# Optimization experiments

Measured on AMD Instinct MI355X. Metric: run time of the kernel, lower is better.

Reference implementation:

```python
import jax, jax.numpy as jnp
import numpy as np

N_HEAD = 16
SCALE = True


def setup_inputs() -> dict:
    key = jax.random.key(0)
    k1, k2, k3 = jax.random.split(key, 3)
    B, S, D = 4, 2048, 1024
    x = jax.random.normal(k1, (B, S, D), dtype=jnp.float32)
    w_attn = jax.random.normal(k2, (D, 3 * D), dtype=jnp.float32) * 0.02
    b_attn = jnp.zeros((3 * D,), dtype=jnp.float32)
    w_proj = jax.random.normal(k3, (D, D), dtype=jnp.float32) * 0.02
    b_proj = jnp.zeros((D,), dtype=jnp.float32)
    return {"x": x, "w_attn": w_attn, "b_attn": b_attn, "w_proj": w_proj, "b_proj": b_proj}


def reference(x, w_attn, b_attn, w_proj, b_proj):
    B, S, D = x.shape
    H = N_HEAD
    hd = D // H
    qkv = x @ w_attn + b_attn  # [B,S,3D] (Conv1D)
    q, k, v = jnp.split(qkv, 3, axis=-1)
    # split heads -> [B,H,S,hd]
    q = q.reshape(B, S, H, hd).transpose(0, 2, 1, 3)
    k = k.reshape(B, S, H, hd).transpose(0, 2, 1, 3)
    v = v.reshape(B, S, H, hd).transpose(0, 2, 1, 3)
    w = jnp.einsum('bhqd,bhkd->bhqk', q, k)  # [B,H,S,S]
    if SCALE:
        w = w / jnp.sqrt(jnp.asarray(hd, dtype=w.dtype))
    # causal mask exactly as in source: w*b + -10000*(1-b)
    bmask = jnp.tril(jnp.ones((S, S), dtype=w.dtype))[None, None]
    w = w * bmask + (-10000.0) * (1.0 - bmask)
    w = jax.nn.softmax(w, axis=-1)
    a = jnp.einsum('bhqk,bhkd->bhqd', w, v)  # [B,H,S,hd]
    a = a.transpose(0, 2, 1, 3).reshape(B, S, D)  # merge heads
    out = a @ w_proj + b_proj
    return out
```

## Files before the change

kernel.cpp:

```cpp
#include <hip/hip_runtime.h>

typedef __attribute__((ext_vector_type(8))) _Float16 f16x8;
typedef __attribute__((ext_vector_type(2))) __fp16 h16x2;
typedef __attribute__((ext_vector_type(4))) float f32x4;

#define S_LEN 2048
#define DMODEL 1024
#define NHEAD 16
#define HD 64
#define QKV_LD 3072
#define BTOT 4
#define LOG2E 1.4426950408889634f

#define GLL16(g, l)                                              \
  __builtin_amdgcn_global_load_lds(                              \
      (const __attribute__((address_space(1))) void*)(g),        \
      (__attribute__((address_space(3))) void*)(l), 16, 0, 0)

#define MFMA16(a, b, c) __builtin_amdgcn_mfma_f32_16x16x32_f16(a, b, c, 0, 0, 0)

__global__ __launch_bounds__(256) void cvt_f32_f16_k(const float* __restrict__ in,
                                                     _Float16* __restrict__ out, int n) {
  int i = (blockIdx.x * 256 + threadIdx.x) * 4;
  int stride = gridDim.x * 256 * 4;
  for (; i < n; i += stride) {
    float4 v = *(const float4*)(in + i);
    _Float16 h[4];
    h[0] = (_Float16)v.x; h[1] = (_Float16)v.y; h[2] = (_Float16)v.z; h[3] = (_Float16)v.w;
    *(uint2*)(out + i) = *(const uint2*)h;
  }
}

__global__ __launch_bounds__(256) void transpose_cvt_k(const float* __restrict__ W,
                                                       _Float16* __restrict__ Wt,
                                                       int K, int N) {
  __shared__ float t[32][33];
  int n0 = blockIdx.x * 32, k0 = blockIdx.y * 32;
  int tx = threadIdx.x, ty = threadIdx.y;
#pragma unroll
  for (int i = 0; i < 32; i += 8)
    t[ty + i][tx] = W[(size_t)(k0 + ty + i) * N + n0 + tx];
  __syncthreads();
#pragma unroll
  for (int i = 0; i < 32; i += 8)
    Wt[(size_t)(n0 + ty + i) * K + k0 + tx] = (_Float16)t[tx][ty + i];
}

template <int OUT_F32>
__global__ __launch_bounds__(256) void gemm_bt_k(const _Float16* __restrict__ A,
                                                 const _Float16* __restrict__ Bt,
                                                 const float* __restrict__ bias,
                                                 void* __restrict__ C,
                                                 int M, int N, int K) {
  __shared__ _Float16 As[128 * 64];
  __shared__ _Float16 Bs[128 * 64];
  const int tid = threadIdx.x;
  const int wid = tid >> 6, lane = tid & 63;
  const int quad = lane >> 4, l16 = lane & 15;
  const int wr = wid >> 1, wc = wid & 1;

  const int lin = blockIdx.y * gridDim.x + blockIdx.x;
  const int width = 8 * gridDim.x;
  const int group = lin / width;
  const int pm = group * 8 + (lin % width) % 8;
  const int pn = (lin % width) / 8;
  const int tm = pm * 128, tn = pn * 128;

  const int row0 = tid >> 3;
  const int xc = 8 * ((tid & 7) ^ (row0 & 7));
  const _Float16* Ag = A + (size_t)(tm + row0) * K + xc;
  const _Float16* Bg = Bt + (size_t)(tn + row0) * K + xc;
  _Float16* AsW = &As[wid * 512];
  _Float16* BsW = &Bs[wid * 512];

  f32x4 acc[4][4] = {};

  for (int k0 = 0; k0 < K; k0 += 64) {
    __syncthreads();
#pragma unroll
    for (int p = 0; p < 4; p++) {
      GLL16(Ag + k0 + (size_t)(32 * p) * K, AsW + 2048 * p);
      GLL16(Bg + k0 + (size_t)(32 * p) * K, BsW + 2048 * p);
    }
    __syncthreads();

#pragma unroll
    for (int ks = 0; ks < 2; ks++) {
      f16x8 af[4], bf[4];
#pragma unroll
      for (int mt = 0; mt < 4; mt++)
        af[mt] = *(const f16x8*)&As[(wr * 64 + mt * 16 + l16) * 64 +
                                    (((ks * 4 + quad) ^ (l16 & 7)) << 3)];
#pragma unroll
      for (int nt = 0; nt < 4; nt++)
        bf[nt] = *(const f16x8*)&Bs[(wc * 64 + nt * 16 + l16) * 64 +
                                    (((ks * 4 + quad) ^ (l16 & 7)) << 3)];
#pragma unroll
      for (int mt = 0; mt < 4; mt++)
#pragma unroll
        for (int nt = 0; nt < 4; nt++)
          acc[mt][nt] = MFMA16(af[mt], bf[nt], acc[mt][nt]);
    }
  }

#pragma unroll
  for (int nt = 0; nt < 4; nt++) {
    int col = tn + wc * 64 + nt * 16 + l16;
    float bv = bias[col];
#pragma unroll
    for (int mt = 0; mt < 4; mt++) {
      int row = tm + wr * 64 + mt * 16 + quad * 4;
#pragma unroll
      for (int r = 0; r < 4; r++) {
        float v = acc[mt][nt][r] + bv;
        if (OUT_F32)
          ((float*)C)[(size_t)(row + r) * N + col] = v;
        else
          ((_Float16*)C)[(size_t)(row + r) * N + col] = (_Float16)v;
      }
    }
  }
}

__global__ __launch_bounds__(256, 3) void attn_k(const _Float16* __restrict__ qkv,
                                                 _Float16* __restrict__ out) {
  __shared__ _Float16 Ks[2][4096];
  __shared__ _Float16 VTs[2][4096];
  __shared__ _Float16 Ps[4][2304];

  const int tid = threadIdx.x, wid = tid >> 6, lane = tid & 63;
  const int quad = lane >> 4, l16 = lane & 15;
  const int bh = blockIdx.x, b = bh >> 4, h = bh & 15;
  const int tile = 15 - blockIdx.y;
  const int qt = tile * 128;
  const _Float16* base = qkv + (size_t)b * S_LEN * QKV_LD + h * HD;

  const int krow = tid >> 3;
  const _Float16* Kg = base + DMODEL + (size_t)krow * QKV_LD +
                       8 * ((tid & 7) ^ (krow & 7));
  const int kp = tid & 31, dbase = (tid >> 5) * 8;
  const _Float16* Vg = base + 2 * DMODEL + (size_t)(2 * kp) * QKV_LD + dbase;

  int voff[8];
#pragma unroll
  for (int i = 0; i < 8; i++) {
    int d = dbase + i;
    voff[i] = d * 32 + (((kp >> 2) ^ (d & 7)) << 2) + (kp & 3);
  }

  auto stage_V = [&](int bufi, uint4 v0, uint4 v1) {
    union { uint4 u; _Float16 h[8]; } a, c;
    a.u = v0; c.u = v1;
    uint* VT32 = (uint*)VTs[bufi];
#pragma unroll
    for (int i = 0; i < 8; i++) {
      union { _Float16 h[2]; uint u; } w;
      w.h[0] = a.h[i]; w.h[1] = c.h[i];
      VT32[voff[i]] = w.u;
    }
  };

  f16x8 bq[2][2];
  {
    const _Float16 qs = (_Float16)(0.125f * LOG2E);
#pragma unroll
    for (int nt = 0; nt < 2; nt++)
#pragma unroll
      for (int ks = 0; ks < 2; ks++) {
        union { uint4 u; f16x8 h; } v;
        v.u = *(const uint4*)(base + (size_t)(qt + wid * 32 + nt * 16 + l16) * QKV_LD +
                              ks * 32 + quad * 8);
        bq[nt][ks] = v.h * qs;
      }
  }

  float m_i[2] = {-1e30f, -1e30f}, l_i[2] = {0.f, 0.f};
  f32x4 o[4][2] = {};

  const int qmin_w = qt + wid * 32;
  const int qmax_w = qmin_w + 31;
  const int nj = qt / 64 + 2;

  GLL16(Kg, &Ks[0][wid * 512]);
  GLL16(Kg + (size_t)32 * QKV_LD, &Ks[0][2048 + wid * 512]);
  stage_V(0, *(const uint4*)(Vg), *(const uint4*)(Vg + QKV_LD));
  __syncthreads();

  for (int j = 0; j < nj; j++) {
    const int cur = j & 1, nxt = cur ^ 1;
    const int k0g = j * 64;
    const bool pf = (j + 1 < nj);
    uint4 pv0, pv1;
    if (pf) {
      const int kn = k0g + 64;
      GLL16(Kg + (size_t)kn * QKV_LD, &Ks[nxt][wid * 512]);
      GLL16(Kg + (size_t)(kn + 32) * QKV_LD, &Ks[nxt][2048 + wid * 512]);
      pv0 = *(const uint4*)(Vg + (size_t)kn * QKV_LD);
      pv1 = *(const uint4*)(Vg + (size_t)(kn + 1) * QKV_LD);
    }

    if (k0g <= qmax_w) {
      f32x4 sc[4][2] = {};
#pragma unroll
      for (int ks = 0; ks < 2; ks++) {
#pragma unroll
        for (int mt = 0; mt < 4; mt++) {
          f16x8 ak = *(const f16x8*)&Ks[cur][(mt * 16 + l16) * 64 +
                                             (((ks * 4 + quad) ^ (l16 & 7)) << 3)];
          sc[mt][0] = MFMA16(ak, bq[0][ks], sc[mt][0]);
          sc[mt][1] = MFMA16(ak, bq[1][ks], sc[mt][1]);
        }
      }

      const bool need_mask = (k0g + 63 > qmin_w);
      float s[2][16];
      float mx[2];
#pragma unroll
      for (int nt = 0; nt < 2; nt++) {
        const int qg = qmin_w + nt * 16 + l16;
#pragma unroll
        for (int mt = 0; mt < 4; mt++)
#pragma unroll
          for (int r = 0; r < 4; r++) {
            float v = sc[mt][nt][r];
            if (need_mask) {
              int kg = k0g + mt * 16 + quad * 4 + r;
              v = (kg <= qg) ? v : -3.0e38f;
            }
            s[nt][mt * 4 + r] = v;
          }
        float t0 = fmaxf(fmaxf(s[nt][0], s[nt][1]), s[nt][2]);
        float t1 = fmaxf(fmaxf(s[nt][3], s[nt][4]), s[nt][5]);
        float t2 = fmaxf(fmaxf(s[nt][6], s[nt][7]), s[nt][8]);
        float t3 = fmaxf(fmaxf(s[nt][9], s[nt][10]), s[nt][11]);
        float t4 = fmaxf(fmaxf(s[nt][12], s[nt][13]), s[nt][14]);
        float m0 = fmaxf(fmaxf(t0, t1), t2);
        float m1 = fmaxf(fmaxf(t3, t4), s[nt][15]);
        float m = fmaxf(m0, m1);
        m = fmaxf(m, __shfl_xor(m, 16, 64));
        m = fmaxf(m, __shfl_xor(m, 32, 64));
        mx[nt] = m;
      }

      bool grow = (mx[0] > m_i[0] + 8.0f) || (mx[1] > m_i[1] + 8.0f);
      if (__any(grow)) {
#pragma unroll
        for (int nt = 0; nt < 2; nt++) {
          float mnew = fmaxf(m_i[nt], mx[nt]);
          float alpha = __builtin_amdgcn_exp2f(m_i[nt] - mnew);
          m_i[nt] = mnew;
          l_i[nt] *= alpha;
#pragma unroll
          for (int md = 0; md < 4; md++) o[md][nt] *= alpha;
        }
      }

#pragma unroll
      for (int nt = 0; nt < 2; nt++) {
        float pe[16];
#pragma unroll
        for (int i = 0; i < 16; i++)
          pe[i] = __builtin_amdgcn_exp2f(s[nt][i] - m_i[nt]);
        float rs = ((pe[0] + pe[1]) + (pe[2] + pe[3])) +
                   ((pe[4] + pe[5]) + (pe[6] + pe[7])) +
                   (((pe[8] + pe[9]) + (pe[10] + pe[11])) +
                    ((pe[12] + pe[13]) + (pe[14] + pe[15])));
        rs += __shfl_xor(rs, 16, 64);
        rs += __shfl_xor(rs, 32, 64);
        l_i[nt] += rs;

#pragma unroll
        for (int mt = 0; mt < 4; mt++) {
          union { h16x2 h[2]; uint2 u; } w;
          w.h[0] = __builtin_amdgcn_cvt_pkrtz(pe[mt * 4 + 0], pe[mt * 4 + 1]);
          w.h[1] = __builtin_amdgcn_cvt_pkrtz(pe[mt * 4 + 2], pe[mt * 4 + 3]);
          *(uint2*)&Ps[wid][(nt * 16 + l16) * 72 + mt * 16 + quad * 4] = w.u;
        }
      }

#pragma unroll
      for (int ks = 0; ks < 2; ks++) {
        f16x8 bp0 = *(const f16x8*)&Ps[wid][l16 * 72 + ks * 32 + quad * 8];
        f16x8 bp1 = *(const f16x8*)&Ps[wid][(16 + l16) * 72 + ks * 32 + quad * 8];
#pragma unroll
        for (int md = 0; md < 4; md++) {
          f16x8 av = *(const f16x8*)&VTs[cur][(md * 16 + l16) * 64 +
                                              (((ks * 4 + quad) ^ (l16 & 7)) << 3)];
          o[md][0] = MFMA16(av, bp0, o[md][0]);
          o[md][1] = MFMA16(av, bp1, o[md][1]);
        }
      }
    }

    if (pf) stage_V(nxt, pv0, pv1);
    __syncthreads();
  }

#pragma unroll
  for (int nt = 0; nt < 2; nt++) {
    float inv = 1.0f / l_i[nt];
#pragma unroll
    for (int md = 0; md < 4; md++) {
      union { h16x2 h[2]; uint2 u; } w;
      w.h[0] = __builtin_amdgcn_cvt_pkrtz(o[md][nt][0] * inv, o[md][nt][1] * inv);
      w.h[1] = __builtin_amdgcn_cvt_pkrtz(o[md][nt][2] * inv, o[md][nt][3] * inv);
      *(uint2*)&Ps[wid][(nt * 16 + l16) * 72 + md * 16 + quad * 4] = w.u;
    }
  }
  {
    int r = lane >> 1, ch = (lane & 1) * 32;
    const int qg = qt + wid * 32 + r;
    _Float16* orow = out + (size_t)(b * S_LEN + qg) * DMODEL + h * HD + ch;
#pragma unroll
    for (int i = 0; i < 4; i++)
      *(uint4*)(orow + i * 8) = *(const uint4*)&Ps[wid][r * 72 + ch + i * 8];
  }
}

extern "C" void kernel_launch(void* const* d_in, const int* in_sizes, int n_in,
                              void* d_out, int out_size, void* d_ws, size_t ws_size,
                              hipStream_t stream) {
  const float* x = (const float*)d_in[0];
  const float* w_attn = (const float*)d_in[1];
  const float* b_attn = (const float*)d_in[2];
  const float* w_proj = (const float*)d_in[3];
  const float* b_proj = (const float*)d_in[4];
  float* outp = (float*)d_out;

  char* ws = (char*)d_ws;
  _Float16* x16 = (_Float16*)ws;
  _Float16* wTa = (_Float16*)(ws + 16777216);
  _Float16* wTp = (_Float16*)(ws + 16777216 + 6291456);
  _Float16* qkv = (_Float16*)(ws + 25165824);
  _Float16* abuf = (_Float16*)(ws + 75497472);

  const int nx = BTOT * S_LEN * DMODEL;

  cvt_f32_f16_k<<<8192, 256, 0, stream>>>(x, x16, nx);
  transpose_cvt_k<<<dim3(QKV_LD / 32, DMODEL / 32), dim3(32, 8), 0, stream>>>(
      w_attn, wTa, DMODEL, QKV_LD);
  transpose_cvt_k<<<dim3(DMODEL / 32, DMODEL / 32), dim3(32, 8), 0, stream>>>(
      w_proj, wTp, DMODEL, DMODEL);

  gemm_bt_k<0><<<dim3(QKV_LD / 128, BTOT * S_LEN / 128), 256, 0, stream>>>(
      x16, wTa, b_attn, qkv, BTOT * S_LEN, QKV_LD, DMODEL);

  attn_k<<<dim3(BTOT * NHEAD, 16), 256, 0, stream>>>(qkv, abuf);

  gemm_bt_k<1><<<dim3(DMODEL / 128, BTOT * S_LEN / 128), 256, 0, stream>>>(
      abuf, wTp, b_proj, outp, BTOT * S_LEN, DMODEL, DMODEL);
}
```

Baseline: 269.6 us.

## Split attention KV across wave groups and pair causal tiles per block

The attention kernel now uses 512 threads per block. Two groups of four waves each handle one 32-key half of every 64-key tile for the same queries, and their partial softmax states are merged through shared memory at the end. Each block also processes two query tiles, p and 15-p, so every block gets a balanced amount of causal work and the grid shrinks to 8 blocks per head. The aim is more waves in flight and an even load across blocks. The cost is an extra merge step, additional barriers, and a larger LDS pool per block, which may cap occupancy.

```diff
diff --git a/kernel.cpp b/kernel.cpp
--- a/kernel.cpp
+++ b/kernel.cpp
@@ -122,23 +122,26 @@
   }
 }
 
-__global__ __launch_bounds__(256, 3) void attn_k(const _Float16* __restrict__ qkv,
+__global__ __launch_bounds__(512, 4) void attn_k(const _Float16* __restrict__ qkv,
                                                  _Float16* __restrict__ out) {
-  __shared__ _Float16 Ks[2][4096];
-  __shared__ _Float16 VTs[2][4096];
-  __shared__ _Float16 Ps[4][2304];
+  __shared__ __align__(16) char pool[54272];
+  _Float16* KsB = (_Float16*)pool;
+  _Float16* VTsB = (_Float16*)(pool + 16384);
+  float* ML = (float*)(pool + 53248);
 
   const int tid = threadIdx.x, wid = tid >> 6, lane = tid & 63;
   const int quad = lane >> 4, l16 = lane & 15;
+  const int qg = wid & 3, kg = wid >> 2;
+  _Float16* PsW = (_Float16*)(pool + 32768) + wid * 1280;
   const int bh = blockIdx.x, b = bh >> 4, h = bh & 15;
-  const int tile = 15 - blockIdx.y;
-  const int qt = tile * 128;
+  const int p = blockIdx.y;
   const _Float16* base = qkv + (size_t)b * S_LEN * QKV_LD + h * HD;
 
   const int krow = tid >> 3;
   const _Float16* Kg = base + DMODEL + (size_t)krow * QKV_LD +
                        8 * ((tid & 7) ^ (krow & 7));
-  const int kp = tid & 31, dbase = (tid >> 5) * 8;
+  const bool vstager = (tid < 256);
+  const int kp = tid & 31, dbase = ((tid >> 5) & 7) * 8;
   const _Float16* Vg = base + 2 * DMODEL + (size_t)(2 * kp) * QKV_LD + dbase;
 
   int voff[8];
@@ -151,7 +154,7 @@
   auto stage_V = [&](int bufi, uint4 v0, uint4 v1) {
     union { uint4 u; _Float16 h[8]; } a, c;
     a.u = v0; c.u = v1;
-    uint* VT32 = (uint*)VTs[bufi];
+    uint* VT32 = (uint*)(VTsB + bufi * 4096);
 #pragma unroll
     for (int i = 0; i < 8; i++) {
       union { _Float16 h[2]; uint u; } w;
@@ -160,161 +163,193 @@
     }
   };
 
-  f16x8 bq[2][2];
-  {
-    const _Float16 qs = (_Float16)(0.125f * LOG2E);
-#pragma unroll
-    for (int nt = 0; nt < 2; nt++)
-#pragma unroll
-      for (int ks = 0; ks < 2; ks++) {
-        union { uint4 u; f16x8 h; } v;
-        v.u = *(const uint4*)(base + (size_t)(qt + wid * 32 + nt * 16 + l16) * QKV_LD +
-                              ks * 32 + quad * 8);
-        bq[nt][ks] = v.h * qs;
-      }
-  }
-
-  float m_i[2] = {-1e30f, -1e30f}, l_i[2] = {0.f, 0.f};
-  f32x4 o[4][2] = {};
-
-  const int qmin_w = qt + wid * 32;
-  const int qmax_w = qmin_w + 31;
-  const int nj = qt / 64 + 2;
-
-  GLL16(Kg, &Ks[0][wid * 512]);
-  GLL16(Kg + (size_t)32 * QKV_LD, &Ks[0][2048 + wid * 512]);
-  stage_V(0, *(const uint4*)(Vg), *(const uint4*)(Vg + QKV_LD));
-  __syncthreads();
-
-  for (int j = 0; j < nj; j++) {
-    const int cur = j & 1, nxt = cur ^ 1;
-    const int k0g = j * 64;
-    const bool pf = (j + 1 < nj);
-    uint4 pv0, pv1;
-    if (pf) {
-      const int kn = k0g + 64;
-      GLL16(Kg + (size_t)kn * QKV_LD, &Ks[nxt][wid * 512]);
-      GLL16(Kg + (size_t)(kn + 32) * QKV_LD, &Ks[nxt][2048 + wid * 512]);
-      pv0 = *(const uint4*)(Vg + (size_t)kn * QKV_LD);
-      pv1 = *(const uint4*)(Vg + (size_t)(kn + 1) * QKV_LD);
-    }
-
-    if (k0g <= qmax_w) {
-      f32x4 sc[4][2] = {};
-#pragma unroll
-      for (int ks = 0; ks < 2; ks++) {
-#pragma unroll
-        for (int mt = 0; mt < 4; mt++) {
-          f16x8 ak = *(const f16x8*)&Ks[cur][(mt * 16 + l16) * 64 +
-                                             (((ks * 4 + quad) ^ (l16 & 7)) << 3)];
-          sc[mt][0] = MFMA16(ak, bq[0][ks], sc[mt][0]);
-          sc[mt][1] = MFMA16(ak, bq[1][ks], sc[mt][1]);
-        }
-      }
-
-      const bool need_mask = (k0g + 63 > qmin_w);
-      float s[2][16];
-      float mx[2];
-#pragma unroll
-      for (int nt = 0; nt < 2; nt++) {
-        const int qg = qmin_w + nt * 16 + l16;
-#pragma unroll
-        for (int mt = 0; mt < 4; mt++)
-#pragma unroll
-          for (int r = 0; r < 4; r++) {
-            float v = sc[mt][nt][r];
-            if (need_mask) {
-              int kg = k0g + mt * 16 + quad * 4 + r;
-              v = (kg <= qg) ? v : -3.0e38f;
+  auto run_pass = [&](int qt) {
+    f16x8 bq[2][2];
+    {
+      const _Float16 qs = (_Float16)(0.125f * LOG2E);
+#pragma unroll
+      for (int nt = 0; nt < 2; nt++)
+#pragma unroll
+        for (int ks = 0; ks < 2; ks++) {
+          union { uint4 u; f16x8 h; } v;
+          v.u = *(const uint4*)(base +
+                                (size_t)(qt + qg * 32 + nt * 16 + l16) * QKV_LD +
+                                ks * 32 + quad * 8);
+          bq[nt][ks] = v.h * qs;
+        }
+    }
+
+    float m_i[2] = {-1e30f, -1e30f}, l_i[2] = {0.f, 0.f};
+    f32x4 o[4][2] = {};
+
+    const int qmin_w = qt + qg * 32;
+    const int qmax_w = qmin_w + 31;
+    const int nj = qt / 64 + 2;
+
+    __syncthreads();
+    GLL16(Kg, KsB + wid * 512);
+    if (vstager) stage_V(0, *(const uint4*)(Vg), *(const uint4*)(Vg + QKV_LD));
+    __syncthreads();
+
+    for (int j = 0; j < nj; j++) {
+      const int cur = j & 1, nxt = cur ^ 1;
+      const int k0g = j * 64;
+      const bool pf = (j + 1 < nj);
+      uint4 pv0, pv1;
+      if (pf) {
+        const int kn = k0g + 64;
+        GLL16(Kg + (size_t)kn * QKV_LD, KsB + nxt * 4096 + wid * 512);
+        if (vstager) {
+          pv0 = *(const uint4*)(Vg + (size_t)kn * QKV_LD);
+          pv1 = *(const uint4*)(Vg + (size_t)(kn + 1) * QKV_LD);
+        }
+      }
+
+      if (k0g <= qmax_w) {
+        const _Float16* Kc = KsB + cur * 4096;
+        f32x4 sc[2][2] = {};
+#pragma unroll
+        for (int ks = 0; ks < 2; ks++)
+#pragma unroll
+          for (int mt = 0; mt < 2; mt++) {
+            f16x8 ak = *(const f16x8*)&Kc[(kg * 32 + mt * 16 + l16) * 64 +
+                                          (((ks * 4 + quad) ^ (l16 & 7)) << 3)];
+            sc[mt][0] = MFMA16(ak, bq[0][ks], sc[mt][0]);
+            sc[mt][1] = MFMA16(ak, bq[1][ks], sc[mt][1]);
+          }
+
+        const int kgbase = k0g + kg * 32;
+        const bool need_mask = (kgbase + 31 > qmin_w);
+        float s[2][8];
+        float mx[2];
+#pragma unroll
+        for (int nt = 0; nt < 2; nt++) {
+          const int qgl = qmin_w + nt * 16 + l16;
+#pragma unroll
+          for (int mt = 0; mt < 2; mt++)
+#pragma unroll
+            for (int r = 0; r < 4; r++) {
+              float v = sc[mt][nt][r];
+              if (need_mask) {
+                int kgi = kgbase + mt * 16 + quad * 4 + r;
+                v = (kgi <= qgl) ? v : -3.0e38f;
+              }
+              s[nt][mt * 4 + r] = v;
             }
-            s[nt][mt * 4 + r] = v;
+          float t0 = fmaxf(fmaxf(s[nt][0], s[nt][1]), s[nt][2]);
+          float t1 = fmaxf(fmaxf(s[nt][3], s[nt][4]), s[nt][5]);
+          float m = fmaxf(fmaxf(t0, t1), fmaxf(s[nt][6], s[nt][7]));
+          m = fmaxf(m, __shfl_xor(m, 16, 64));
+          m = fmaxf(m, __shfl_xor(m, 32, 64));
+          mx[nt] = m;
+        }
+
+        bool grow = (mx[0] > m_i[0] + 8.0f) || (mx[1] > m_i[1] + 8.0f);
+        if (__any(grow)) {
+#pragma unroll
+          for (int nt = 0; nt < 2; nt++) {
+            float mnew = fmaxf(m_i[nt], mx[nt]);
+            float alpha = __builtin_amdgcn_exp2f(m_i[nt] - mnew);
+            m_i[nt] = mnew;
+            l_i[nt] *= alpha;
+#pragma unroll
+            for (int md = 0; md < 4; md++) o[md][nt] *= alpha;
           }
-        float t0 = fmaxf(fmaxf(s[nt][0], s[nt][1]), s[nt][2]);
-        float t1 = fmaxf(fmaxf(s[nt][3], s[nt][4]), s[nt][5]);
-        float t2 = fmaxf(fmaxf(s[nt][6], s[nt][7]), s[nt][8]);
-        float t3 = fmaxf(fmaxf(s[nt][9], s[nt][10]), s[nt][11]);
-        float t4 = fmaxf(fmaxf(s[nt][12], s[nt][13]), s[nt][14]);
-        float m0 = fmaxf(fmaxf(t0, t1), t2);
-        float m1 = fmaxf(fmaxf(t3, t4), s[nt][15]);
-        float m = fmaxf(m0, m1);
-        m = fmaxf(m, __shfl_xor(m, 16, 64));
-        m = fmaxf(m, __shfl_xor(m, 32, 64));
-        mx[nt] = m;
-      }
-
-      bool grow = (mx[0] > m_i[0] + 8.0f) || (mx[1] > m_i[1] + 8.0f);
-      if (__any(grow)) {
+        }
+
 #pragma unroll
         for (int nt = 0; nt < 2; nt++) {
-          float mnew = fmaxf(m_i[nt], mx[nt]);
-          float alpha = __builtin_amdgcn_exp2f(m_i[nt] - mnew);
-          m_i[nt] = mnew;
-          l_i[nt] *= alpha;
-#pragma unroll
-          for (int md = 0; md < 4; md++) o[md][nt] *= alpha;
-        }
-      }
-
-#pragma unroll
-      for (int nt = 0; nt < 2; nt++) {
-        float pe[16];
-#pragma unroll
-        for (int i = 0; i < 16; i++)
-          pe[i] = __builtin_amdgcn_exp2f(s[nt][i] - m_i[nt]);
-        float rs = ((pe[0] + pe[1]) + (pe[2] + pe[3])) +
-                   ((pe[4] + pe[5]) + (pe[6] + pe[7])) +
-                   (((pe[8] + pe[9]) + (pe[10] + pe[11])) +
-                    ((pe[12] + pe[13]) + (pe[14] + pe[15])));
-        rs += __shfl_xor(rs, 16, 64);
-        rs += __shfl_xor(rs, 32, 64);
-        l_i[nt] += rs;
-
-#pragma unroll
-        for (int mt = 0; mt < 4; mt++) {
-          union { h16x2 h[2]; uint2 u; } w;
-          w.h[0] = __builtin_amdgcn_cvt_pkrtz(pe[mt * 4 + 0], pe[mt * 4 + 1]);
-          w.h[1] = __builtin_amdgcn_cvt_pkrtz(pe[mt * 4 + 2], pe[mt * 4 + 3]);
-          *(uint2*)&Ps[wid][(nt * 16 + l16) * 72 + mt * 16 + quad * 4] = w.u;
-        }
-      }
-
-#pragma unroll
-      for (int ks = 0; ks < 2; ks++) {
-        f16x8 bp0 = *(const f16x8*)&Ps[wid][l16 * 72 + ks * 32 + quad * 8];
-        f16x8 bp1 = *(const f16x8*)&Ps[wid][(16 + l16) * 72 + ks * 32 + quad * 8];
+          float pe[8];
+#pragma unroll
+          for (int i = 0; i < 8; i++)
+            pe[i] = __builtin_amdgcn_exp2f(s[nt][i] - m_i[nt]);
+          l_i[nt] += ((pe[0] + pe[1]) + (pe[2] + pe[3])) +
+                     ((pe[4] + pe[5]) + (pe[6] + pe[7]));
+#pragma unroll
+          for (int mt = 0; mt < 2; mt++) {
+            union { h16x2 h[2]; uint2 u; } w;
+            w.h[0] = __builtin_amdgcn_cvt_pkrtz(pe[mt * 4 + 0], pe[mt * 4 + 1]);
+            w.h[1] = __builtin_amdgcn_cvt_pkrtz(pe[mt * 4 + 2], pe[mt * 4 + 3]);
+            *(uint2*)&PsW[(nt * 16 + l16) * 40 + mt * 16 + quad * 4] = w.u;
+          }
+        }
+
+        const _Float16* Vc = VTsB + cur * 4096;
+        f16x8 bp0 = *(const f16x8*)&PsW[l16 * 40 + quad * 8];
+        f16x8 bp1 = *(const f16x8*)&PsW[(16 + l16) * 40 + quad * 8];
 #pragma unroll
         for (int md = 0; md < 4; md++) {
-          f16x8 av = *(const f16x8*)&VTs[cur][(md * 16 + l16) * 64 +
-                                              (((ks * 4 + quad) ^ (l16 & 7)) << 3)];
+          f16x8 av = *(const f16x8*)&Vc[(md * 16 + l16) * 64 +
+                                        (((kg * 4 + quad) ^ (l16 & 7)) << 3)];
           o[md][0] = MFMA16(av, bp0, o[md][0]);
           o[md][1] = MFMA16(av, bp1, o[md][1]);
         }
       }
-    }
-
-    if (pf) stage_V(nxt, pv0, pv1);
-    __syncthreads();
-  }
-
-#pragma unroll
-  for (int nt = 0; nt < 2; nt++) {
-    float inv = 1.0f / l_i[nt];
-#pragma unroll
-    for (int md = 0; md < 4; md++) {
-      union { h16x2 h[2]; uint2 u; } w;
-      w.h[0] = __builtin_amdgcn_cvt_pkrtz(o[md][nt][0] * inv, o[md][nt][1] * inv);
-      w.h[1] = __builtin_amdgcn_cvt_pkrtz(o[md][nt][2] * inv, o[md][nt][3] * inv);
-      *(uint2*)&Ps[wid][(nt * 16 + l16) * 72 + md * 16 + quad * 4] = w.u;
-    }
-  }
-  {
-    int r = lane >> 1, ch = (lane & 1) * 32;
-    const int qg = qt + wid * 32 + r;
-    _Float16* orow = out + (size_t)(b * S_LEN + qg) * DMODEL + h * HD + ch;
-#pragma unroll
-    for (int i = 0; i < 4; i++)
-      *(uint4*)(orow + i * 8) = *(const uint4*)&Ps[wid][r * 72 + ch + i * 8];
-  }
+
+      if (pf && vstager) stage_V(nxt, pv0, pv1);
+      __syncthreads();
+    }
+
+#pragma unroll
+    for (int nt = 0; nt < 2; nt++) {
+      float r = l_i[nt];
+      r += __shfl_xor(r, 16, 64);
+      r += __shfl_xor(r, 32, 64);
+      l_i[nt] = r;
+    }
+    float* X = (float*)pool;
+    if (kg == 1) {
+#pragma unroll
+      for (int md = 0; md < 4; md++)
+#pragma unroll
+        for (int nt = 0; nt < 2; nt++)
+          *(f32x4*)&X[qg * 2048 + (md * 2 + nt) * 256 + lane * 4] = o[md][nt];
+      if (quad == 0) {
+#pragma unroll
+        for (int nt = 0; nt < 2; nt++) {
+          ML[((qg * 2 + nt) * 2 + 0) * 16 + l16] = m_i[nt];
+          ML[((qg * 2 + nt) * 2 + 1) * 16 + l16] = l_i[nt];
+        }
+      }
+    }
+    __syncthreads();
+    if (kg == 0) {
+      _Float16* PsE = (_Float16*)(pool + 32768) + qg * 2304;
+      float w0[2], w1[2], inv[2];
+#pragma unroll
+      for (int nt = 0; nt < 2; nt++) {
+        float m1 = ML[((qg * 2 + nt) * 2 + 0) * 16 + l16];
+        float l1 = ML[((qg * 2 + nt) * 2 + 1) * 16 + l16];
+        float mm = fmaxf(m_i[nt], m1);
+        w0[nt] = __builtin_amdgcn_exp2f(m_i[nt] - mm);
+        w1[nt] = __builtin_amdgcn_exp2f(m1 - mm);
+        float lt = l_i[nt] * w0[nt] + l1 * w1[nt];
+        inv[nt] = 1.0f / lt;
+      }
+#pragma unroll
+      for (int md = 0; md < 4; md++)
+#pragma unroll
+        for (int nt = 0; nt < 2; nt++) {
+          f32x4 o1 = *(const f32x4*)&X[qg * 2048 + (md * 2 + nt) * 256 + lane * 4];
+          f32x4 ot = o[md][nt] * w0[nt] + o1 * w1[nt];
+          union { h16x2 h[2]; uint2 u; } w;
+          w.h[0] = __builtin_amdgcn_cvt_pkrtz(ot[0] * inv[nt], ot[1] * inv[nt]);
+          w.h[1] = __builtin_amdgcn_cvt_pkrtz(ot[2] * inv[nt], ot[3] * inv[nt]);
+          *(uint2*)&PsE[(nt * 16 + l16) * 72 + md * 16 + quad * 4] = w.u;
+        }
+      {
+        int r = lane >> 1, ch = (lane & 1) * 32;
+        const int qgl = qt + qg * 32 + r;
+        _Float16* orow = out + (size_t)(b * S_LEN + qgl) * DMODEL + h * HD + ch;
+#pragma unroll
+        for (int i = 0; i < 4; i++)
+          *(uint4*)(orow + i * 8) = *(const uint4*)&PsE[r * 72 + ch + i * 8];
+      }
+    }
+  };
+
+  run_pass(p * 128);
+  run_pass((15 - p) * 128);
 }
 
 extern "C" void kernel_launch(void* const* d_in, const int* in_sizes, int n_in,
@@ -345,7 +380,7 @@
   gemm_bt_k<0><<<dim3(QKV_LD / 128, BTOT * S_LEN / 128), 256, 0, stream>>>(
       x16, wTa, b_attn, qkv, BTOT * S_LEN, QKV_LD, DMODEL);
 
-  attn_k<<<dim3(BTOT * NHEAD, 16), 256, 0, stream>>>(qkv, abuf);
+  attn_k<<<dim3(BTOT * NHEAD, 8), 512, 0, stream>>>(qkv, abuf);
 
   gemm_bt_k<1><<<dim3(DMODEL / 128, BTOT * S_LEN / 128), 256, 0, stream>>>(
       abuf, wTp, b_proj, outp, BTOT * S_LEN, DMODEL, DMODEL);
```

Result: no change. 266.9 us (-1.0%).
